# Optimization experiments

Measured on AMD Instinct MI355X. Metric: run time of the kernel, lower is better.

## Reference

```python
import jax, jax.numpy as jnp
import numpy as np

EPSILON = 1e-05
B, H, P, T, D = 256, 8, 64, 3, 64

def setup_inputs() -> dict:
    key = jax.random.key(0)
    ks = jax.random.split(key, 7)
    return {
        "X": jax.random.normal(ks[0], (B, H, P, T), dtype=jnp.float32),
        "W_left": jax.random.normal(ks[1], (H, P, D), dtype=jnp.float32),
        "W_right": jax.random.normal(ks[2], (H, P, D), dtype=jnp.float32),
        "fc1_w": jax.random.normal(ks[3], (D, H * P * D), dtype=jnp.float32) / np.sqrt(H * P * D),
        "fc1_b": jax.random.normal(ks[4], (D,), dtype=jnp.float32) * 0.01,
        "fc2_w": jax.random.normal(ks[5], (1, D), dtype=jnp.float32) / np.sqrt(D),
        "fc2_b": jax.random.normal(ks[6], (1,), dtype=jnp.float32) * 0.01,
    }

def reference(X, W_left, W_right, fc1_w, fc1_b, fc2_w, fc2_b):
    # pairwise deltas: [B,h,i,j,t]
    delta = X[..., :, None, :] - X[..., None, :, :]
    # relu(delta^2) is a no-op mathematically but kept faithful
    distance = jnp.sqrt(jnp.maximum(delta * delta, 0.0) + EPSILON)
    dX = (delta / distance) * jnp.exp(-distance)  # direction * exp(-dist)
    Xl = jnp.einsum('nhijt,hjd->nhidt', dX, W_left)
    Xr = jnp.einsum('nhijt,hjd->nhidt', dX, W_right)
    att = jnp.einsum('nhidt,nhidt->nhid', Xl, Xr)  # reduce over t
    flat = att.reshape(att.shape[0], -1)  # [B, h*p*d]
    hdn = jax.nn.silu(flat @ fc1_w.T + fc1_b)
    return hdn @ fc2_w.T + fc2_b  # [B, 1]
```

## Files before the change

kernel.cpp:

```cpp
#include <hip/hip_runtime.h>
#include <hip/hip_bf16.h>


typedef __attribute__((ext_vector_type(8))) short short8;
typedef __attribute__((ext_vector_type(4))) float f32x4;

#define PADW 72
#define PADM 1032
#define KTOT 32768L

__device__ __forceinline__ unsigned short f2b(float x) {
  union { float f; unsigned int u; } v; v.f = x;
  return (unsigned short)((v.u + 0x7FFFu + ((v.u >> 16) & 1u)) >> 16);
}

__device__ __forceinline__ unsigned int pk_bf16(float a, float b) {
  unsigned int r;
  asm("v_cvt_pk_bf16_f32 %0, %1, %2" : "=v"(r) : "v"(a), "v"(b));
  return r;
}

__global__ __launch_bounds__(512, 4)
void k_fused(const float* __restrict__ X, const float* __restrict__ Wl_g,
             const float* __restrict__ Wr_g,
             const float* __restrict__ fc1w,
             float* __restrict__ partial) {
  __shared__ float xs[16][3][64];
  __shared__ __align__(16) union {
    struct {
      unsigned short wl[64][PADW];
      unsigned short wr[64][PADW];
      unsigned short dxs[2][3][16][PADW];
    } a;
    float red[8][16][64];
  } u;
  __shared__ __align__(16) unsigned short att_s[16][PADM];

  const int blk  = blockIdx.x;
  const int sl   = ((blk >> 7) << 3) | (blk & 7);
  const int iq   = sl & 3;
  const int h    = sl >> 2;
  const int ng   = (blk >> 3) & 15;
  const int tid  = threadIdx.x;
  const int lane = tid & 63;
  const int w    = tid >> 6;
  const int c0   = lane & 15;
  const int ks   = lane >> 4;
  const int qsub = w & 1;
  const int dblk = w >> 1;

  const float* wlg = Wl_g + h * 4096;
  const float* wrg = Wr_g + h * 4096;
#pragma unroll
  for (int r = 0; r < 8; ++r) {
    int e = tid + r * 512;
    int j = e >> 6, d = e & 63;
    u.a.wl[d][j] = f2b(wlg[e]);
    u.a.wr[d][j] = f2b(wrg[e]);
  }
  {
    const long xbase = ((long)(ng * 16) * 8 + h) * 192;
#pragma unroll
    for (int r = 0; r < 6; ++r) {
      int e = tid + r * 512;
      int q = e / 192;
      int rem = e - q * 192;
      int i = rem / 3;
      int t = rem - i * 3;
      xs[q][t][i] = X[xbase + (long)q * 1536 + rem];
    }
  }
  __syncthreads();

  short8 bl[2], br[2];
#pragma unroll
  for (int kb = 0; kb < 2; ++kb) {
    const int d = dblk * 16 + c0;
    const int j0 = ks * 8 + 32 * kb;
    bl[kb] = *(const short8*)&u.a.wl[d][j0];
    br[kb] = *(const short8*)&u.a.wr[d][j0];
  }

  const int dq = tid >> 8;
  const int il = (tid >> 4) & 15;
  const int j4 = (tid & 15) << 2;

  for (int it = 0; it < 8; ++it) {
    const int qd = it * 2 + dq;
    if (it) __syncthreads();
#pragma unroll
    for (int t = 0; t < 3; ++t) {
      const float xi = xs[qd][t][iq * 16 + il];
      float d0 = xi - xs[qd][t][j4];
      float d1 = xi - xs[qd][t][j4 + 1];
      float d2 = xi - xs[qd][t][j4 + 2];
      float d3 = xi - xs[qd][t][j4 + 3];
      float s0 = d0 * d0 + 1e-5f, s1 = d1 * d1 + 1e-5f;
      float s2 = d2 * d2 + 1e-5f, s3 = d3 * d3 + 1e-5f;
      float i0 = __builtin_amdgcn_rsqf(s0), i1 = __builtin_amdgcn_rsqf(s1);
      float i2 = __builtin_amdgcn_rsqf(s2), i3 = __builtin_amdgcn_rsqf(s3);
      float e0 = __builtin_amdgcn_exp2f(-1.44269504f * (s0 * i0));
      float e1 = __builtin_amdgcn_exp2f(-1.44269504f * (s1 * i1));
      float e2 = __builtin_amdgcn_exp2f(-1.44269504f * (s2 * i2));
      float e3 = __builtin_amdgcn_exp2f(-1.44269504f * (s3 * i3));
      *(unsigned int*)&u.a.dxs[dq][t][il][j4] =
          pk_bf16(d0 * i0 * e0, d1 * i1 * e1);
      *(unsigned int*)&u.a.dxs[dq][t][il][j4 + 2] =
          pk_bf16(d2 * i2 * e2, d3 * i3 * e3);
    }
    __syncthreads();

    const int q = it * 2 + qsub;
    f32x4 acc;
    acc[0] = 0.f; acc[1] = 0.f; acc[2] = 0.f; acc[3] = 0.f;
#pragma unroll
    for (int t = 0; t < 3; ++t) {
      short8 a0 = *(const short8*)&u.a.dxs[qsub][t][c0][ks * 8];
      short8 a1 = *(const short8*)&u.a.dxs[qsub][t][c0][ks * 8 + 32];
      f32x4 xl; xl[0]=0.f; xl[1]=0.f; xl[2]=0.f; xl[3]=0.f;
      f32x4 xr; xr[0]=0.f; xr[1]=0.f; xr[2]=0.f; xr[3]=0.f;
      xl = __builtin_amdgcn_mfma_f32_16x16x32_bf16(a0, bl[0], xl, 0, 0, 0);
      xl = __builtin_amdgcn_mfma_f32_16x16x32_bf16(a1, bl[1], xl, 0, 0, 0);
      xr = __builtin_amdgcn_mfma_f32_16x16x32_bf16(a0, br[0], xr, 0, 0, 0);
      xr = __builtin_amdgcn_mfma_f32_16x16x32_bf16(a1, br[1], xr, 0, 0, 0);
      acc += xl * xr;
    }
#pragma unroll
    for (int r = 0; r < 4; ++r)
      att_s[q][(ks * 4 + r) * 64 + dblk * 16 + c0] = f2b(acc[r]);
  }
  __syncthreads();

  f32x4 facc[4];
#pragma unroll
  for (int cb = 0; cb < 4; ++cb) {
    facc[cb][0] = 0.f; facc[cb][1] = 0.f; facc[cb][2] = 0.f; facc[cb][3] = 0.f;
  }
  const float* bpf =
      fc1w + (long)c0 * KTOT + h * 4096 + iq * 1024 + w * 128 + ks * 8;
  const unsigned short* ap = &att_s[0][0] + c0 * PADM + w * 128 + ks * 8;
#pragma unroll
  for (int s = 0; s < 4; ++s) {
    short8 a = *(const short8*)(ap + s * 32);
#pragma unroll
    for (int cb = 0; cb < 4; ++cb) {
      const float* src = bpf + (long)cb * 16 * KTOT + s * 32;
      f32x4 v0 = *(const f32x4*)(src);
      f32x4 v1 = *(const f32x4*)(src + 4);
      union { unsigned short us[8]; short8 s8; } pw;
      pw.us[0] = f2b(v0[0]);
      pw.us[1] = f2b(v0[1]);
      pw.us[2] = f2b(v0[2]);
      pw.us[3] = f2b(v0[3]);
      pw.us[4] = f2b(v1[0]);
      pw.us[5] = f2b(v1[1]);
      pw.us[6] = f2b(v1[2]);
      pw.us[7] = f2b(v1[3]);
      facc[cb] = __builtin_amdgcn_mfma_f32_16x16x32_bf16(a, pw.s8, facc[cb], 0, 0, 0);
    }
  }
  __syncthreads();
#pragma unroll
  for (int cb = 0; cb < 4; ++cb)
#pragma unroll
    for (int r = 0; r < 4; ++r)
      u.red[w][ks * 4 + r][c0 + 16 * cb] = facc[cb][r];
  __syncthreads();
#pragma unroll
  for (int rep = 0; rep < 2; ++rep) {
    int e = tid + rep * 512;
    int nl = e >> 6, k = e & 63;
    float s = 0.f;
#pragma unroll
    for (int ww = 0; ww < 8; ++ww) s += u.red[ww][nl][k];
    partial[(((long)h * 4 + iq) * 256 + ng * 16 + nl) * 64 + k] = s;
  }
}

__global__ __launch_bounds__(256)
void k_fc2(const float* __restrict__ partial, const float* __restrict__ fc1_b,
           const float* __restrict__ fc2_w, const float* __restrict__ fc2_b,
           float* __restrict__ out) {
  const int tid = threadIdx.x;
  const int n = blockIdx.x * 4 + (tid >> 6);
  const int k = tid & 63;
  float s = fc1_b[k];
#pragma unroll
  for (int sp = 0; sp < 32; ++sp)
    s += partial[((long)sp * 256 + n) * 64 + k];
  float g = s / (1.f + __expf(-s));
  float v = g * fc2_w[k];
#pragma unroll
  for (int off = 32; off > 0; off >>= 1)
    v += __shfl_xor(v, off, 64);
  if (k == 0) out[n] = v + fc2_b[0];
}

extern "C" void kernel_launch(void* const* d_in, const int* in_sizes, int n_in,
                              void* d_out, int out_size, void* d_ws, size_t ws_size,
                              hipStream_t stream) {
  const float* X    = (const float*)d_in[0];
  const float* Wl   = (const float*)d_in[1];
  const float* Wr   = (const float*)d_in[2];
  const float* fc1w = (const float*)d_in[3];
  const float* fc1b = (const float*)d_in[4];
  const float* fc2w = (const float*)d_in[5];
  const float* fc2b = (const float*)d_in[6];
  float* out = (float*)d_out;

  float* partial = (float*)d_ws;

  hipLaunchKernelGGL(k_fused, dim3(512), dim3(512), 0, stream, X, Wl, Wr, fc1w, partial);
  hipLaunchKernelGGL(k_fc2,   dim3(64), dim3(256), 0, stream, partial, fc1b, fc2w, fc2b, out);
}
```

Before: 32.77 us.

## Fuse fc2 epilogue into main kernel via atomic completion counter

Removes the separate fc2 kernel launch. Each block bumps a global atomic counter when it finishes. The last 8 blocks to arrive spin until all 512 have finished, then each computes the fc1 bias, SiLU and fc2 reduction for 32 batch rows. The counter is cleared with a memset before launch. This saves one kernel launch gap, but adds a memset node and spin-waiting that depends on all blocks being co-resident or already completed.

```diff
diff --git a/kernel.cpp b/kernel.cpp
--- a/kernel.cpp
+++ b/kernel.cpp
@@ -24,7 +24,10 @@
 void k_fused(const float* __restrict__ X, const float* __restrict__ Wl_g,
              const float* __restrict__ Wr_g,
              const float* __restrict__ fc1w,
-             float* __restrict__ partial) {
+             const float* __restrict__ fc1b, const float* __restrict__ fc2w,
+             const float* __restrict__ fc2b,
+             float* __restrict__ partial, unsigned int* __restrict__ counter,
+             float* __restrict__ out) {
   __shared__ float xs[16][3][64];
   __shared__ __align__(16) union {
     struct {
@@ -35,6 +38,7 @@
     float red[8][16][64];
   } u;
   __shared__ __align__(16) unsigned short att_s[16][PADM];
+  __shared__ unsigned int ord_s;
 
   const int blk  = blockIdx.x;
   const int sl   = ((blk >> 7) << 3) | (blk & 7);
@@ -175,25 +179,39 @@
     for (int ww = 0; ww < 8; ++ww) s += u.red[ww][nl][k];
     partial[(((long)h * 4 + iq) * 256 + ng * 16 + nl) * 64 + k] = s;
   }
-}
-
-__global__ __launch_bounds__(256)
-void k_fc2(const float* __restrict__ partial, const float* __restrict__ fc1_b,
-           const float* __restrict__ fc2_w, const float* __restrict__ fc2_b,
-           float* __restrict__ out) {
-  const int tid = threadIdx.x;
-  const int n = blockIdx.x * 4 + (tid >> 6);
-  const int k = tid & 63;
-  float s = fc1_b[k];
-#pragma unroll
-  for (int sp = 0; sp < 32; ++sp)
-    s += partial[((long)sp * 256 + n) * 64 + k];
-  float g = s / (1.f + __expf(-s));
-  float v = g * fc2_w[k];
-#pragma unroll
-  for (int off = 32; off > 0; off >>= 1)
-    v += __shfl_xor(v, off, 64);
-  if (k == 0) out[n] = v + fc2_b[0];
+
+  __syncthreads();
+  if (tid == 0) {
+    __threadfence();
+    unsigned int old = atomicAdd(counter, 1u);
+    ord_s = old;
+    if (old >= 504u) {
+      while (__hip_atomic_load(counter, __ATOMIC_ACQUIRE,
+                               __HIP_MEMORY_SCOPE_AGENT) < 512u) {
+        __builtin_amdgcn_s_sleep(8);
+      }
+    }
+  }
+  __syncthreads();
+  const unsigned int ord = ord_s;
+  if (ord < 504u) return;
+
+  const int slice = (int)(ord - 504u);
+  const int k = lane;
+#pragma unroll
+  for (int r = 0; r < 4; ++r) {
+    const int n = slice * 32 + w * 4 + r;
+    float s = fc1b[k];
+#pragma unroll
+    for (int sp = 0; sp < 32; ++sp)
+      s += partial[((long)sp * 256 + n) * 64 + k];
+    float g = s / (1.f + __expf(-s));
+    float v = g * fc2w[k];
+#pragma unroll
+    for (int off = 32; off > 0; off >>= 1)
+      v += __shfl_xor(v, off, 64);
+    if (k == 0) out[n] = v + fc2b[0];
+  }
 }
 
 extern "C" void kernel_launch(void* const* d_in, const int* in_sizes, int n_in,
@@ -208,8 +226,11 @@
   const float* fc2b = (const float*)d_in[6];
   float* out = (float*)d_out;
 
-  float* partial = (float*)d_ws;
-
-  hipLaunchKernelGGL(k_fused, dim3(512), dim3(512), 0, stream, X, Wl, Wr, fc1w, partial);
-  hipLaunchKernelGGL(k_fc2,   dim3(64), dim3(256), 0, stream, partial, fc1b, fc2w, fc2b, out);
-}
+  char* ws = (char*)d_ws;
+  float*        partial = (float*)ws;
+  unsigned int* counter = (unsigned int*)(ws + 2097152);
+
+  hipMemsetAsync(counter, 0, 4, stream);
+  hipLaunchKernelGGL(k_fused, dim3(512), dim3(512), 0, stream,
+                     X, Wl, Wr, fc1w, fc1b, fc2w, fc2b, partial, counter, out);
+}
```

Result: slower. 55.54 us (+69.5%).

## Compute dX fragments in registers per wave, removing LDS staging and barriers

Applied to the files above, without the earlier changes.

Each wave now computes the bf16 dX MFMA A-operand directly in registers from x values in LDS, instead of staging dX through shared memory with two barriers per iteration. Each wave owns two batch rows and all four d-blocks, and keeps all W_left/W_right B fragments in registers (16 short8). This removes 16 block-wide syncs and the dX LDS round trip. In exchange the transcendental work per element is no longer shared across waves in the same layout, register pressure rises under the 4-blocks-per-SIMD launch bound, and the per-element bf16 conversion uses the software f2b routine instead of the packed hardware convert.

```diff
diff --git a/kernel.cpp b/kernel.cpp
--- a/kernel.cpp
+++ b/kernel.cpp
@@ -14,10 +14,12 @@
   return (unsigned short)((v.u + 0x7FFFu + ((v.u >> 16) & 1u)) >> 16);
 }
 
-__device__ __forceinline__ unsigned int pk_bf16(float a, float b) {
-  unsigned int r;
-  asm("v_cvt_pk_bf16_f32 %0, %1, %2" : "=v"(r) : "v"(a), "v"(b));
-  return r;
+__device__ __forceinline__ unsigned short dxval(float xi, float xj) {
+  float d = xi - xj;
+  float s = d * d + 1e-5f;
+  float iv = __builtin_amdgcn_rsqf(s);
+  float e = __builtin_amdgcn_exp2f(-1.44269504f * (s * iv));
+  return f2b(d * iv * e);
 }
 
 __global__ __launch_bounds__(512, 4)
@@ -26,15 +28,12 @@
              const float* __restrict__ fc1w,
              float* __restrict__ partial) {
   __shared__ float xs[16][3][64];
+  __shared__ __align__(16) unsigned short wl[64][PADW];
+  __shared__ __align__(16) unsigned short wr[64][PADW];
   __shared__ __align__(16) union {
-    struct {
-      unsigned short wl[64][PADW];
-      unsigned short wr[64][PADW];
-      unsigned short dxs[2][3][16][PADW];
-    } a;
+    unsigned short att[16][PADM];
     float red[8][16][64];
-  } u;
-  __shared__ __align__(16) unsigned short att_s[16][PADM];
+  } s;
 
   const int blk  = blockIdx.x;
   const int sl   = ((blk >> 7) << 3) | (blk & 7);
@@ -46,8 +45,6 @@
   const int w    = tid >> 6;
   const int c0   = lane & 15;
   const int ks   = lane >> 4;
-  const int qsub = w & 1;
-  const int dblk = w >> 1;
 
   const float* wlg = Wl_g + h * 4096;
   const float* wrg = Wr_g + h * 4096;
@@ -55,8 +52,8 @@
   for (int r = 0; r < 8; ++r) {
     int e = tid + r * 512;
     int j = e >> 6, d = e & 63;
-    u.a.wl[d][j] = f2b(wlg[e]);
-    u.a.wr[d][j] = f2b(wrg[e]);
+    wl[d][j] = f2b(wlg[e]);
+    wr[d][j] = f2b(wrg[e]);
   }
   {
     const long xbase = ((long)(ng * 16) * 8 + h) * 192;
@@ -72,62 +69,57 @@
   }
   __syncthreads();
 
-  short8 bl[2], br[2];
-#pragma unroll
-  for (int kb = 0; kb < 2; ++kb) {
-    const int d = dblk * 16 + c0;
-    const int j0 = ks * 8 + 32 * kb;
-    bl[kb] = *(const short8*)&u.a.wl[d][j0];
-    br[kb] = *(const short8*)&u.a.wr[d][j0];
-  }
-
-  const int dq = tid >> 8;
-  const int il = (tid >> 4) & 15;
-  const int j4 = (tid & 15) << 2;
-
-  for (int it = 0; it < 8; ++it) {
-    const int qd = it * 2 + dq;
-    if (it) __syncthreads();
+  short8 bl[4][2], br[4][2];
+#pragma unroll
+  for (int cb = 0; cb < 4; ++cb)
+#pragma unroll
+    for (int kb = 0; kb < 2; ++kb) {
+      const int d = cb * 16 + c0;
+      const int j0 = ks * 8 + 32 * kb;
+      bl[cb][kb] = *(const short8*)&wl[d][j0];
+      br[cb][kb] = *(const short8*)&wr[d][j0];
+    }
+
+#pragma unroll
+  for (int qq = 0; qq < 2; ++qq) {
+    const int q = 2 * w + qq;
+    f32x4 acc[4];
+#pragma unroll
+    for (int cb = 0; cb < 4; ++cb) {
+      acc[cb][0] = 0.f; acc[cb][1] = 0.f; acc[cb][2] = 0.f; acc[cb][3] = 0.f;
+    }
 #pragma unroll
     for (int t = 0; t < 3; ++t) {
-      const float xi = xs[qd][t][iq * 16 + il];
-      float d0 = xi - xs[qd][t][j4];
-      float d1 = xi - xs[qd][t][j4 + 1];
-      float d2 = xi - xs[qd][t][j4 + 2];
-      float d3 = xi - xs[qd][t][j4 + 3];
-      float s0 = d0 * d0 + 1e-5f, s1 = d1 * d1 + 1e-5f;
-      float s2 = d2 * d2 + 1e-5f, s3 = d3 * d3 + 1e-5f;
-      float i0 = __builtin_amdgcn_rsqf(s0), i1 = __builtin_amdgcn_rsqf(s1);
-      float i2 = __builtin_amdgcn_rsqf(s2), i3 = __builtin_amdgcn_rsqf(s3);
-      float e0 = __builtin_amdgcn_exp2f(-1.44269504f * (s0 * i0));
-      float e1 = __builtin_amdgcn_exp2f(-1.44269504f * (s1 * i1));
-      float e2 = __builtin_amdgcn_exp2f(-1.44269504f * (s2 * i2));
-      float e3 = __builtin_amdgcn_exp2f(-1.44269504f * (s3 * i3));
-      *(unsigned int*)&u.a.dxs[dq][t][il][j4] =
-          pk_bf16(d0 * i0 * e0, d1 * i1 * e1);
-      *(unsigned int*)&u.a.dxs[dq][t][il][j4 + 2] =
-          pk_bf16(d2 * i2 * e2, d3 * i3 * e3);
-    }
-    __syncthreads();
-
-    const int q = it * 2 + qsub;
-    f32x4 acc;
-    acc[0] = 0.f; acc[1] = 0.f; acc[2] = 0.f; acc[3] = 0.f;
-#pragma unroll
-    for (int t = 0; t < 3; ++t) {
-      short8 a0 = *(const short8*)&u.a.dxs[qsub][t][c0][ks * 8];
-      short8 a1 = *(const short8*)&u.a.dxs[qsub][t][c0][ks * 8 + 32];
-      f32x4 xl; xl[0]=0.f; xl[1]=0.f; xl[2]=0.f; xl[3]=0.f;
-      f32x4 xr; xr[0]=0.f; xr[1]=0.f; xr[2]=0.f; xr[3]=0.f;
-      xl = __builtin_amdgcn_mfma_f32_16x16x32_bf16(a0, bl[0], xl, 0, 0, 0);
-      xl = __builtin_amdgcn_mfma_f32_16x16x32_bf16(a1, bl[1], xl, 0, 0, 0);
-      xr = __builtin_amdgcn_mfma_f32_16x16x32_bf16(a0, br[0], xr, 0, 0, 0);
-      xr = __builtin_amdgcn_mfma_f32_16x16x32_bf16(a1, br[1], xr, 0, 0, 0);
-      acc += xl * xr;
-    }
-#pragma unroll
-    for (int r = 0; r < 4; ++r)
-      att_s[q][(ks * 4 + r) * 64 + dblk * 16 + c0] = f2b(acc[r]);
+      const float* xrow = &xs[q][t][0];
+      const float xi = xrow[iq * 16 + c0];
+      f32x4 xa = *(const f32x4*)(xrow + ks * 8);
+      f32x4 xb = *(const f32x4*)(xrow + ks * 8 + 4);
+      f32x4 xc = *(const f32x4*)(xrow + ks * 8 + 32);
+      f32x4 xd = *(const f32x4*)(xrow + ks * 8 + 36);
+      union { unsigned short us[8]; short8 s8; } A0, A1;
+#pragma unroll
+      for (int e = 0; e < 4; ++e) {
+        A0.us[e]     = dxval(xi, xa[e]);
+        A0.us[4 + e] = dxval(xi, xb[e]);
+        A1.us[e]     = dxval(xi, xc[e]);
+        A1.us[4 + e] = dxval(xi, xd[e]);
+      }
+#pragma unroll
+      for (int cb = 0; cb < 4; ++cb) {
+        f32x4 xl; xl[0]=0.f; xl[1]=0.f; xl[2]=0.f; xl[3]=0.f;
+        f32x4 xr; xr[0]=0.f; xr[1]=0.f; xr[2]=0.f; xr[3]=0.f;
+        xl = __builtin_amdgcn_mfma_f32_16x16x32_bf16(A0.s8, bl[cb][0], xl, 0, 0, 0);
+        xl = __builtin_amdgcn_mfma_f32_16x16x32_bf16(A1.s8, bl[cb][1], xl, 0, 0, 0);
+        xr = __builtin_amdgcn_mfma_f32_16x16x32_bf16(A0.s8, br[cb][0], xr, 0, 0, 0);
+        xr = __builtin_amdgcn_mfma_f32_16x16x32_bf16(A1.s8, br[cb][1], xr, 0, 0, 0);
+        acc[cb] += xl * xr;
+      }
+    }
+#pragma unroll
+    for (int cb = 0; cb < 4; ++cb)
+#pragma unroll
+      for (int r = 0; r < 4; ++r)
+        s.att[q][(ks * 4 + r) * 64 + cb * 16 + c0] = f2b(acc[cb][r]);
   }
   __syncthreads();
 
@@ -138,13 +130,13 @@
   }
   const float* bpf =
       fc1w + (long)c0 * KTOT + h * 4096 + iq * 1024 + w * 128 + ks * 8;
-  const unsigned short* ap = &att_s[0][0] + c0 * PADM + w * 128 + ks * 8;
-#pragma unroll
-  for (int s = 0; s < 4; ++s) {
-    short8 a = *(const short8*)(ap + s * 32);
+  const unsigned short* ap = &s.att[0][0] + c0 * PADM + w * 128 + ks * 8;
+#pragma unroll
+  for (int sx = 0; sx < 4; ++sx) {
+    short8 a = *(const short8*)(ap + sx * 32);
 #pragma unroll
     for (int cb = 0; cb < 4; ++cb) {
-      const float* src = bpf + (long)cb * 16 * KTOT + s * 32;
+      const float* src = bpf + (long)cb * 16 * KTOT + sx * 32;
       f32x4 v0 = *(const f32x4*)(src);
       f32x4 v1 = *(const f32x4*)(src + 4);
       union { unsigned short us[8]; short8 s8; } pw;
@@ -164,16 +156,16 @@
   for (int cb = 0; cb < 4; ++cb)
 #pragma unroll
     for (int r = 0; r < 4; ++r)
-      u.red[w][ks * 4 + r][c0 + 16 * cb] = facc[cb][r];
+      s.red[w][ks * 4 + r][c0 + 16 * cb] = facc[cb][r];
   __syncthreads();
 #pragma unroll
   for (int rep = 0; rep < 2; ++rep) {
     int e = tid + rep * 512;
     int nl = e >> 6, k = e & 63;
-    float s = 0.f;
-#pragma unroll
-    for (int ww = 0; ww < 8; ++ww) s += u.red[ww][nl][k];
-    partial[(((long)h * 4 + iq) * 256 + ng * 16 + nl) * 64 + k] = s;
+    float sum = 0.f;
+#pragma unroll
+    for (int ww = 0; ww < 8; ++ww) sum += s.red[ww][nl][k];
+    partial[(((long)h * 4 + iq) * 256 + ng * 16 + nl) * 64 + k] = sum;
   }
 }
 
```

Result: no change. 32.17 us (median of 2 runs) (-1.8%).

## Shrink LDS footprint with streamed X double-buffer and union att buffer

Applied to the files above, without the earlier changes.

Instead of preloading all 16 batch rows of X into shared memory, the kernel now streams two rows per iteration into a double buffer, prefetching the next pair during compute. It moves the attention staging buffer into the union with the weight tiles and reduction scratch, and raises the launch-bounds occupancy hint from 4 to 6 blocks per CU. The aim is to cut LDS usage so more blocks fit per CU and to hide X load latency. In exchange it adds per-iteration global loads, an extra barrier after the weight fragments are read, and possibly more register pressure under the tighter bound.

```diff
diff --git a/kernel.cpp b/kernel.cpp
--- a/kernel.cpp
+++ b/kernel.cpp
@@ -20,21 +20,21 @@
   return r;
 }
 
-__global__ __launch_bounds__(512, 4)
+__global__ __launch_bounds__(512, 6)
 void k_fused(const float* __restrict__ X, const float* __restrict__ Wl_g,
              const float* __restrict__ Wr_g,
              const float* __restrict__ fc1w,
              float* __restrict__ partial) {
-  __shared__ float xs[16][3][64];
+  __shared__ float xsc[2][2][3][64];
+  __shared__ __align__(16) unsigned short dxs[2][3][16][PADW];
   __shared__ __align__(16) union {
     struct {
       unsigned short wl[64][PADW];
       unsigned short wr[64][PADW];
-      unsigned short dxs[2][3][16][PADW];
-    } a;
+    } w;
+    unsigned short att[16][PADM];
     float red[8][16][64];
-  } u;
-  __shared__ __align__(16) unsigned short att_s[16][PADM];
+  } s;
 
   const int blk  = blockIdx.x;
   const int sl   = ((blk >> 7) << 3) | (blk & 7);
@@ -55,20 +55,13 @@
   for (int r = 0; r < 8; ++r) {
     int e = tid + r * 512;
     int j = e >> 6, d = e & 63;
-    u.a.wl[d][j] = f2b(wlg[e]);
-    u.a.wr[d][j] = f2b(wrg[e]);
-  }
-  {
-    const long xbase = ((long)(ng * 16) * 8 + h) * 192;
-#pragma unroll
-    for (int r = 0; r < 6; ++r) {
-      int e = tid + r * 512;
-      int q = e / 192;
-      int rem = e - q * 192;
-      int i = rem / 3;
-      int t = rem - i * 3;
-      xs[q][t][i] = X[xbase + (long)q * 1536 + rem];
-    }
+    s.w.wl[d][j] = f2b(wlg[e]);
+    s.w.wr[d][j] = f2b(wrg[e]);
+  }
+  const long xrow0 = ((long)(ng * 16) * 8 + h) * 192;
+  if (tid < 384) {
+    int qd = tid / 192, rem = tid - qd * 192;
+    xsc[0][qd][rem % 3][rem / 3] = X[xrow0 + (long)qd * 1536 + rem];
   }
   __syncthreads();
 
@@ -77,24 +70,30 @@
   for (int kb = 0; kb < 2; ++kb) {
     const int d = dblk * 16 + c0;
     const int j0 = ks * 8 + 32 * kb;
-    bl[kb] = *(const short8*)&u.a.wl[d][j0];
-    br[kb] = *(const short8*)&u.a.wr[d][j0];
-  }
+    bl[kb] = *(const short8*)&s.w.wl[d][j0];
+    br[kb] = *(const short8*)&s.w.wr[d][j0];
+  }
+  __syncthreads();
 
   const int dq = tid >> 8;
   const int il = (tid >> 4) & 15;
   const int j4 = (tid & 15) << 2;
 
   for (int it = 0; it < 8; ++it) {
-    const int qd = it * 2 + dq;
-    if (it) __syncthreads();
+    const int buf = it & 1;
+    if (it < 7 && tid < 384) {
+      int qd = tid / 192, rem = tid - qd * 192;
+      int q = 2 * (it + 1) + qd;
+      xsc[buf ^ 1][qd][rem % 3][rem / 3] = X[xrow0 + (long)q * 1536 + rem];
+    }
 #pragma unroll
     for (int t = 0; t < 3; ++t) {
-      const float xi = xs[qd][t][iq * 16 + il];
-      float d0 = xi - xs[qd][t][j4];
-      float d1 = xi - xs[qd][t][j4 + 1];
-      float d2 = xi - xs[qd][t][j4 + 2];
-      float d3 = xi - xs[qd][t][j4 + 3];
+      const float* xrow = &xsc[buf][dq][t][0];
+      const float xi = xrow[iq * 16 + il];
+      float d0 = xi - xrow[j4];
+      float d1 = xi - xrow[j4 + 1];
+      float d2 = xi - xrow[j4 + 2];
+      float d3 = xi - xrow[j4 + 3];
       float s0 = d0 * d0 + 1e-5f, s1 = d1 * d1 + 1e-5f;
       float s2 = d2 * d2 + 1e-5f, s3 = d3 * d3 + 1e-5f;
       float i0 = __builtin_amdgcn_rsqf(s0), i1 = __builtin_amdgcn_rsqf(s1);
@@ -103,9 +102,9 @@
       float e1 = __builtin_amdgcn_exp2f(-1.44269504f * (s1 * i1));
       float e2 = __builtin_amdgcn_exp2f(-1.44269504f * (s2 * i2));
       float e3 = __builtin_amdgcn_exp2f(-1.44269504f * (s3 * i3));
-      *(unsigned int*)&u.a.dxs[dq][t][il][j4] =
+      *(unsigned int*)&dxs[dq][t][il][j4] =
           pk_bf16(d0 * i0 * e0, d1 * i1 * e1);
-      *(unsigned int*)&u.a.dxs[dq][t][il][j4 + 2] =
+      *(unsigned int*)&dxs[dq][t][il][j4 + 2] =
           pk_bf16(d2 * i2 * e2, d3 * i3 * e3);
     }
     __syncthreads();
@@ -115,8 +114,8 @@
     acc[0] = 0.f; acc[1] = 0.f; acc[2] = 0.f; acc[3] = 0.f;
 #pragma unroll
     for (int t = 0; t < 3; ++t) {
-      short8 a0 = *(const short8*)&u.a.dxs[qsub][t][c0][ks * 8];
-      short8 a1 = *(const short8*)&u.a.dxs[qsub][t][c0][ks * 8 + 32];
+      short8 a0 = *(const short8*)&dxs[qsub][t][c0][ks * 8];
+      short8 a1 = *(const short8*)&dxs[qsub][t][c0][ks * 8 + 32];
       f32x4 xl; xl[0]=0.f; xl[1]=0.f; xl[2]=0.f; xl[3]=0.f;
       f32x4 xr; xr[0]=0.f; xr[1]=0.f; xr[2]=0.f; xr[3]=0.f;
       xl = __builtin_amdgcn_mfma_f32_16x16x32_bf16(a0, bl[0], xl, 0, 0, 0);
@@ -127,7 +126,8 @@
     }
 #pragma unroll
     for (int r = 0; r < 4; ++r)
-      att_s[q][(ks * 4 + r) * 64 + dblk * 16 + c0] = f2b(acc[r]);
+      s.att[q][(ks * 4 + r) * 64 + dblk * 16 + c0] = f2b(acc[r]);
+    if (it < 7) __syncthreads();
   }
   __syncthreads();
 
@@ -138,13 +138,13 @@
   }
   const float* bpf =
       fc1w + (long)c0 * KTOT + h * 4096 + iq * 1024 + w * 128 + ks * 8;
-  const unsigned short* ap = &att_s[0][0] + c0 * PADM + w * 128 + ks * 8;
-#pragma unroll
-  for (int s = 0; s < 4; ++s) {
-    short8 a = *(const short8*)(ap + s * 32);
+  const unsigned short* ap = &s.att[0][0] + c0 * PADM + w * 128 + ks * 8;
+#pragma unroll
+  for (int sx = 0; sx < 4; ++sx) {
+    short8 a = *(const short8*)(ap + sx * 32);
 #pragma unroll
     for (int cb = 0; cb < 4; ++cb) {
-      const float* src = bpf + (long)cb * 16 * KTOT + s * 32;
+      const float* src = bpf + (long)cb * 16 * KTOT + sx * 32;
       f32x4 v0 = *(const f32x4*)(src);
       f32x4 v1 = *(const f32x4*)(src + 4);
       union { unsigned short us[8]; short8 s8; } pw;
@@ -164,16 +164,16 @@
   for (int cb = 0; cb < 4; ++cb)
 #pragma unroll
     for (int r = 0; r < 4; ++r)
-      u.red[w][ks * 4 + r][c0 + 16 * cb] = facc[cb][r];
+      s.red[w][ks * 4 + r][c0 + 16 * cb] = facc[cb][r];
   __syncthreads();
 #pragma unroll
   for (int rep = 0; rep < 2; ++rep) {
     int e = tid + rep * 512;
     int nl = e >> 6, k = e & 63;
-    float s = 0.f;
-#pragma unroll
-    for (int ww = 0; ww < 8; ++ww) s += u.red[ww][nl][k];
-    partial[(((long)h * 4 + iq) * 256 + ng * 16 + nl) * 64 + k] = s;
+    float sum = 0.f;
+#pragma unroll
+    for (int ww = 0; ww < 8; ++ww) sum += s.red[ww][nl][k];
+    partial[(((long)h * 4 + iq) * 256 + ng * 16 + nl) * 64 + k] = sum;
   }
 }
 
```

Measured after the change: 36.32 us. 10.8% more time.
